# Performance work log

Hardware: AMD Instinct MI355X
Metric: run time of the kernel (lower is better)

Reference implementation:

```python
import jax, jax.numpy as jnp
import numpy as np

N_HEADS = 16
D_EMBED = 1024
D_CROSS = 768
D_HEAD = D_EMBED // N_HEADS
B, S = 4, 2048


def setup_inputs() -> dict:
    key = jax.random.key(0)
    ks = jax.random.split(key, 10)
    sq = lambda k, shp, fan: jax.random.normal(k, shp, jnp.float32) / np.sqrt(fan)
    return {
        "x": jax.random.normal(ks[0], (B, S, D_EMBED), jnp.float32),
        "y": jax.random.normal(ks[1], (B, S, D_CROSS), jnp.float32),
        "Wq": sq(ks[2], (D_EMBED, D_EMBED), D_EMBED),
        "bq": jnp.zeros((D_EMBED,), jnp.float32),
        "Wk": sq(ks[3], (D_CROSS, D_EMBED), D_CROSS),
        "bk": jnp.zeros((D_EMBED,), jnp.float32),
        "Wv": sq(ks[4], (D_CROSS, D_EMBED), D_CROSS),
        "bv": jnp.zeros((D_EMBED,), jnp.float32),
        "Wo": sq(ks[5], (D_EMBED, D_EMBED), D_EMBED),
        "bo": jnp.zeros((D_EMBED,), jnp.float32),
    }


def reference(x, y, Wq, bq, Wk, bk, Wv, bv, Wo, bo):
    b, s, _ = y.shape
    q = x @ Wq + bq  # [b, s, d_embed]
    k = y @ Wk + bk
    v = y @ Wv + bv
    # [b, h, s, d_head]
    q = q.reshape(b, s, N_HEADS, D_HEAD).transpose(0, 2, 1, 3)
    k = k.reshape(b, s, N_HEADS, D_HEAD).transpose(0, 2, 1, 3)
    v = v.reshape(b, s, N_HEADS, D_HEAD).transpose(0, 2, 1, 3)
    scale = 1.0 / np.sqrt(D_HEAD).astype(np.float32)
    scores = jnp.einsum("bhqd,bhkd->bhqk", q, k) * scale
    weights = jax.nn.softmax(scores, axis=-1)
    out = jnp.einsum("bhqk,bhkd->bhqd", weights, v)
    out = out.transpose(0, 2, 1, 3).reshape(x.shape)
    return out @ Wo + bo
```

## Files before the change

kernel.cpp:

```cpp
#include <hip/hip_runtime.h>

#define NHEADS 16
#define DEMBED 1024
#define DCROSS 768
#define DHEAD  64
#define BATCH  4
#define SLEN   2048
#define MROWS  (BATCH * SLEN)

using bf16   = __bf16;
using bf16x8 = __attribute__((ext_vector_type(8))) __bf16;
using bf16x4 = __attribute__((ext_vector_type(4))) __bf16;
using bf16x2 = __attribute__((ext_vector_type(2))) __bf16;
using f32x4  = __attribute__((ext_vector_type(4))) float;
using f32x16 = __attribute__((ext_vector_type(16))) float;

__device__ __forceinline__ f32x4 mfma_bf16(bf16x8 a, bf16x8 b, f32x4 c) {
    return __builtin_amdgcn_mfma_f32_16x16x32_bf16(a, b, c, 0, 0, 0);
}
__device__ __forceinline__ f32x16 mfma32(bf16x8 a, bf16x8 b, f32x16 c) {
    return __builtin_amdgcn_mfma_f32_32x32x16_bf16(a, b, c, 0, 0, 0);
}

__device__ __forceinline__ void gl2lds16(const void* g, void* l) {
    __builtin_amdgcn_global_load_lds(
        (const __attribute__((address_space(1))) void*)g,
        (__attribute__((address_space(3))) void*)l, 16, 0, 0);
}

struct PrepArgs {
    const float* wsrc[4]; bf16* wdst[4]; int wK[4];
    const float *x, *y; bf16 *xb, *yb;
};
#define NTRB 4096
__global__ void prep_all(PrepArgs a) {
    const int bid = blockIdx.x;
    const int tid = threadIdx.x;
    if (bid < NTRB) {
        __shared__ float tile[32][33];
        const int which = bid >> 10, rem = bid & 1023;
        const int K = a.wK[which], N = DEMBED;
        const int n0 = (rem & 31) * 32, k0 = (rem >> 5) * 32;
        if (k0 >= K) return;
        const float* W = a.wsrc[which];
        bf16* Wt = a.wdst[which];
        const int tx = tid & 31, ty = tid >> 5;
#pragma unroll
        for (int i = 0; i < 32; i += 8)
            tile[ty + i][tx] = W[(size_t)(k0 + ty + i) * N + n0 + tx];
        __syncthreads();
#pragma unroll
        for (int i = 0; i < 32; i += 8)
            Wt[(size_t)(n0 + ty + i) * K + k0 + tx] = (bf16)tile[tx][ty + i];
    } else {
        const int n4x = MROWS * DEMBED / 4;
        const int n4y = MROWS * DCROSS / 4;
        int i = (bid - NTRB) * 256 + tid;
        const float* src; bf16* dst; int j;
        if (i < n4x) { src = a.x; dst = a.xb; j = i; }
        else { j = i - n4x; if (j >= n4y) return; src = a.y; dst = a.yb; }
        float4 v = ((const float4*)src)[j];
        bf16x4 o = { (bf16)v.x, (bf16)v.y, (bf16)v.z, (bf16)v.w };
        ((bf16x4*)dst)[j] = o;
    }
}

struct QkvArgs {
    const bf16 *xb, *yb, *Wqt, *Wkt, *Wvt;
    const float *bq, *bk, *bv;
    bf16 *Qb, *Kb, *Vt;
    float qscale;
};
__global__ __launch_bounds__(256, 3) void gemm_qkv(QkvArgs a) {
    __shared__ bf16 As[128 * 64];
    __shared__ bf16 Bs[128 * 64];
    const int id = blockIdx.x;
    const int cls = id >> 9;
    const bf16 *A, *Bt;
    const float* bias;
    int K, m0, n0;
    if (cls == 0) { int t = id;        m0 = (t >> 3) * 128; n0 = (t & 7) * 128;
                    A = a.xb;  Bt = a.Wqt; bias = a.bq; K = DEMBED; }
    else if (cls == 1) { int t = id - 512;  m0 = (t >> 3) * 128; n0 = (t & 7) * 128;
                    A = a.yb;  Bt = a.Wkt; bias = a.bk; K = DCROSS; }
    else { int t = id - 1024; m0 = (t >> 6) * 128; n0 = (t & 63) * 128;
                    A = a.Wvt; Bt = a.yb;  bias = a.bv; K = DCROSS; }

    const int tid  = threadIdx.x;
    const int wave = tid >> 6, lane = tid & 63;
    const int quad = lane >> 4, l15 = lane & 15;
    const int wr = wave >> 1, wc = wave & 1;

    const int srow = wave * 8 + (lane >> 3);
    const int scol = ((lane & 7) ^ (lane >> 3)) * 8;
    char* ldsA0 = (char*)As + wave * 1024;
    char* ldsB0 = (char*)Bs + wave * 1024;
    const bf16* gA0 = A + (size_t)(m0 + srow) * K + scol;
    const bf16* gB0 = Bt + (size_t)(n0 + srow) * K + scol;

    const int sw = l15 & 7;

    f32x4 acc[4][4] = {};

    for (int kt = 0; kt < K; kt += 64) {
        __syncthreads();
#pragma unroll
        for (int c = 0; c < 4; c++)
            gl2lds16(gA0 + (size_t)c * 32 * K + kt, ldsA0 + c * 4096);
#pragma unroll
        for (int c = 0; c < 4; c++)
            gl2lds16(gB0 + (size_t)c * 32 * K + kt, ldsB0 + c * 4096);
        __syncthreads();

#pragma unroll
        for (int kg = 0; kg < 2; kg++) {
            bf16x8 af[4], bfr[4];
#pragma unroll
            for (int i = 0; i < 4; i++)
                af[i] = *(const bf16x8*)((const char*)As +
                         (wr * 64 + i * 16 + l15) * 128 + (((kg * 4 + quad) ^ sw) * 16));
#pragma unroll
            for (int i = 0; i < 4; i++)
                bfr[i] = *(const bf16x8*)((const char*)Bs +
                         (wc * 64 + i * 16 + l15) * 128 + (((kg * 4 + quad) ^ sw) * 16));
#pragma unroll
            for (int fr = 0; fr < 4; fr++)
#pragma unroll
                for (int fc = 0; fc < 4; fc++)
                    acc[fr][fc] = mfma_bf16(af[fr], bfr[fc], acc[fr][fc]);
        }
    }

    if (cls < 2) {
        bf16* Cout = (cls == 0) ? a.Qb : a.Kb;
        const float alpha = (cls == 0) ? a.qscale : 1.0f;
#pragma unroll
        for (int fr = 0; fr < 4; fr++) {
            int row = m0 + wr * 64 + fr * 16 + quad * 4;
#pragma unroll
            for (int fc = 0; fc < 4; fc++) {
                int col = n0 + wc * 64 + fc * 16 + l15;
                float bv = bias[col];
#pragma unroll
                for (int r = 0; r < 4; r++)
                    Cout[(size_t)(row + r) * DEMBED + col] =
                        (bf16)((acc[fr][fc][r] + bv) * alpha);
            }
        }
    } else {
        const int b = n0 >> 11;
        const size_t bbase = (size_t)b * DEMBED * SLEN;
#pragma unroll
        for (int fr = 0; fr < 4; fr++) {
            int row = m0 + wr * 64 + fr * 16 + quad * 4;
#pragma unroll
            for (int fc = 0; fc < 4; fc++) {
                int col = n0 + wc * 64 + fc * 16 + l15;
                int s = col & (SLEN - 1);
#pragma unroll
                for (int r = 0; r < 4; r++)
                    a.Vt[bbase + (size_t)(row + r) * SLEN + s] =
                        (bf16)(acc[fr][fc][r] + bias[row + r]);
            }
        }
    }
}

__global__ __launch_bounds__(256, 3) void gemm_o(const bf16* __restrict__ A,
                                                 const bf16* __restrict__ Bt,
                                                 const float* __restrict__ bias,
                                                 float* __restrict__ Cout) {
    const int K = DEMBED, N = DEMBED;
    __shared__ bf16 As[128 * 64];
    __shared__ bf16 Bs[128 * 64];
    const int tid  = threadIdx.x;
    const int wave = tid >> 6, lane = tid & 63;
    const int quad = lane >> 4, l15 = lane & 15;
    const int m0 = blockIdx.x * 128, n0 = blockIdx.y * 128;
    const int wr = wave >> 1, wc = wave & 1;

    const int srow = wave * 8 + (lane >> 3);
    const int scol = ((lane & 7) ^ (lane >> 3)) * 8;
    char* ldsA0 = (char*)As + wave * 1024;
    char* ldsB0 = (char*)Bs + wave * 1024;
    const bf16* gA0 = A + (size_t)(m0 + srow) * K + scol;
    const bf16* gB0 = Bt + (size_t)(n0 + srow) * K + scol;

    const int sw = l15 & 7;

    f32x4 acc[4][4] = {};

    for (int kt = 0; kt < K; kt += 64) {
        __syncthreads();
#pragma unroll
        for (int c = 0; c < 4; c++)
            gl2lds16(gA0 + (size_t)c * 32 * K + kt, ldsA0 + c * 4096);
#pragma unroll
        for (int c = 0; c < 4; c++)
            gl2lds16(gB0 + (size_t)c * 32 * K + kt, ldsB0 + c * 4096);
        __syncthreads();

#pragma unroll
        for (int kg = 0; kg < 2; kg++) {
            bf16x8 af[4], bfr[4];
#pragma unroll
            for (int i = 0; i < 4; i++)
                af[i] = *(const bf16x8*)((const char*)As +
                         (wr * 64 + i * 16 + l15) * 128 + (((kg * 4 + quad) ^ sw) * 16));
#pragma unroll
            for (int i = 0; i < 4; i++)
                bfr[i] = *(const bf16x8*)((const char*)Bs +
                         (wc * 64 + i * 16 + l15) * 128 + (((kg * 4 + quad) ^ sw) * 16));
#pragma unroll
            for (int fr = 0; fr < 4; fr++)
#pragma unroll
                for (int fc = 0; fc < 4; fc++)
                    acc[fr][fc] = mfma_bf16(af[fr], bfr[fc], acc[fr][fc]);
        }
    }

#pragma unroll
    for (int fr = 0; fr < 4; fr++) {
        int row = m0 + wr * 64 + fr * 16 + quad * 4;
#pragma unroll
        for (int fc = 0; fc < 4; fc++) {
            int col = n0 + wc * 64 + fc * 16 + l15;
            float bv = bias[col];
#pragma unroll
            for (int r = 0; r < 4; r++)
                Cout[(size_t)(row + r) * N + col] = acc[fr][fc][r] + bv;
        }
    }
}

__global__ __launch_bounds__(256, 4) void attn(const bf16* __restrict__ Q,
                                               const bf16* __restrict__ K,
                                               const bf16* __restrict__ Vt,
                                               bf16* __restrict__ O) {
    __shared__ bf16 KsA[2][64 * 64];
    __shared__ bf16 VsA[2][64 * 64];

    const int tid  = threadIdx.x;
    const int wave = tid >> 6, lane = tid & 63;
    const int l31  = lane & 31, H = lane >> 5;
    const int bh = blockIdx.x, b = bh >> 4, h = bh & 15;
    const size_t rowbase = (size_t)b * SLEN;
    const int qb = blockIdx.y * 128 + wave * 32;
    const int hc = h * DHEAD;

    bf16x8 qf[4];
#pragma unroll
    for (int ks = 0; ks < 4; ks++)
        qf[ks] = *(const bf16x8*)(Q + (rowbase + qb + l31) * DEMBED
                                  + hc + ks * 16 + H * 8);

    f32x16 o[2] = {};
    float lsv = 0.0f;

    const bf16* Kbase = K + rowbase * DEMBED + hc;
    const bf16* Vbase = Vt + (size_t)bh * DHEAD * SLEN;

    const int xcol = (((tid & 7) ^ ((tid >> 3) & 7)) * 8);
    const bf16* gK = Kbase + (size_t)(tid >> 3) * DEMBED + xcol;
    const bf16* gV = Vbase + (size_t)(tid >> 3) * SLEN + xcol;

    const int swz = l31 & 7;

    {
        char* lk = (char*)KsA + wave * 1024;
        char* lv = (char*)VsA + wave * 1024;
        gl2lds16(gK, lk);
        gl2lds16(gK + (size_t)32 * DEMBED, lk + 32 * 128);
        gl2lds16(gV, lv);
        gl2lds16(gV + 32 * SLEN, lv + 32 * 128);
    }
    __syncthreads();

    int cur = 0;
    for (int kb = 0; kb < SLEN; kb += 64) {
        if (kb + 64 < SLEN) {
            char* lk = (char*)KsA + (cur ^ 1) * 8192 + wave * 1024;
            char* lv = (char*)VsA + (cur ^ 1) * 8192 + wave * 1024;
            gl2lds16(gK + (size_t)(kb + 64) * DEMBED, lk);
            gl2lds16(gK + (size_t)(kb + 96) * DEMBED, lk + 32 * 128);
            gl2lds16(gV + kb + 64, lv);
            gl2lds16(gV + 32 * SLEN + kb + 64, lv + 32 * 128);
        }

        const char* Kbuf = (const char*)KsA + cur * 8192;
        const char* Vbuf = (const char*)VsA + cur * 8192;

        f32x16 s0 = {}, s1 = {};
#pragma unroll
        for (int ks = 0; ks < 4; ks++) {
            bf16x8 kf0 = *(const bf16x8*)(Kbuf + l31 * 128
                          + (((2 * ks + H) ^ swz) * 16));
            bf16x8 kf1 = *(const bf16x8*)(Kbuf + (32 + l31) * 128
                          + (((2 * ks + H) ^ swz) * 16));
            s0 = mfma32(kf0, qf[ks], s0);
            s1 = mfma32(kf1, qf[ks], s1);
        }

        int c0[8], c1[8];
#pragma unroll
        for (int t = 0; t < 8; t++) {
            float a0 = __builtin_amdgcn_exp2f(s0[2 * t]);
            float a1 = __builtin_amdgcn_exp2f(s0[2 * t + 1]);
            float b0 = __builtin_amdgcn_exp2f(s1[2 * t]);
            float b1 = __builtin_amdgcn_exp2f(s1[2 * t + 1]);
            lsv += (a0 + a1) + (b0 + b1);
            union { bf16x2 h; int i; } p0, p1;
            p0.h[0] = (bf16)a0; p0.h[1] = (bf16)a1;
            p1.h[0] = (bf16)b0; p1.h[1] = (bf16)b1;
            c0[t] = p0.i;
            c1[t] = p1.i;
        }

#pragma unroll
        for (int ks = 0; ks < 4; ks++) {
            const int* cc = (ks < 2) ? c0 : c1;
            const int ksl = ks & 1;
            auto w0 = __builtin_amdgcn_permlane32_swap(cc[4 * ksl + 0],
                                                       cc[4 * ksl + 2], false, false);
            auto w1 = __builtin_amdgcn_permlane32_swap(cc[4 * ksl + 1],
                                                       cc[4 * ksl + 3], false, false);
            union { int i[4]; bf16x8 v; } ap;
            ap.i[0] = w0[0]; ap.i[1] = w1[0]; ap.i[2] = w0[1]; ap.i[3] = w1[1];
#pragma unroll
            for (int dg = 0; dg < 2; dg++) {
                bf16x8 vf = *(const bf16x8*)(Vbuf + (dg * 32 + l31) * 128
                              + (((2 * ks + H) ^ swz) * 16));
                o[dg] = mfma32(ap.v, vf, o[dg]);
            }
        }

        __syncthreads();
        cur ^= 1;
    }

    lsv += __shfl_xor(lsv, 32);
    float inv = 1.0f / lsv;
#pragma unroll
    for (int r = 0; r < 16; r++) {
        const int ql = (r & 3) + 8 * (r >> 2) + 4 * H;
        float iv = __shfl(inv, ql);
#pragma unroll
        for (int dg = 0; dg < 2; dg++)
            O[(rowbase + qb + ql) * DEMBED + hc + dg * 32 + l31] =
                (bf16)(o[dg][r] * iv);
    }
}

extern "C" void kernel_launch(void* const* d_in, const int* in_sizes, int n_in,
                              void* d_out, int out_size, void* d_ws, size_t ws_size,
                              hipStream_t stream) {
    const float* x  = (const float*)d_in[0];
    const float* y  = (const float*)d_in[1];
    const float* Wq = (const float*)d_in[2];
    const float* bq = (const float*)d_in[3];
    const float* Wk = (const float*)d_in[4];
    const float* bk = (const float*)d_in[5];
    const float* Wv = (const float*)d_in[6];
    const float* bv = (const float*)d_in[7];
    const float* Wo = (const float*)d_in[8];
    const float* bo = (const float*)d_in[9];
    float* out = (float*)d_out;

    char* ws = (char*)d_ws;
    size_t off = 0;
    auto alloc = [&](size_t bytes) {
        void* p = ws + off;
        off += (bytes + 255) & ~(size_t)255;
        return p;
    };
    bf16* xb  = (bf16*)alloc((size_t)MROWS * DEMBED * 2);
    bf16* yb  = (bf16*)alloc((size_t)MROWS * DCROSS * 2);
    bf16* Wqt = (bf16*)alloc((size_t)DEMBED * DEMBED * 2);
    bf16* Wkt = (bf16*)alloc((size_t)DEMBED * DCROSS * 2);
    bf16* Wvt = (bf16*)alloc((size_t)DEMBED * DCROSS * 2);
    bf16* Wot = (bf16*)alloc((size_t)DEMBED * DEMBED * 2);
    bf16* Qb  = (bf16*)alloc((size_t)MROWS * DEMBED * 2);
    bf16* Kb  = (bf16*)alloc((size_t)MROWS * DEMBED * 2);
    bf16* Vtb = (bf16*)alloc((size_t)MROWS * DEMBED * 2);
    bf16* Ab  = (bf16*)alloc((size_t)MROWS * DEMBED * 2);
    if (off > ws_size) return;

    {
        PrepArgs a;
        a.wsrc[0] = Wq; a.wdst[0] = Wqt; a.wK[0] = DEMBED;
        a.wsrc[1] = Wk; a.wdst[1] = Wkt; a.wK[1] = DCROSS;
        a.wsrc[2] = Wv; a.wdst[2] = Wvt; a.wK[2] = DCROSS;
        a.wsrc[3] = Wo; a.wdst[3] = Wot; a.wK[3] = DEMBED;
        a.x = x; a.y = y; a.xb = xb; a.yb = yb;
        int ncvt = (MROWS * DEMBED / 4 + MROWS * DCROSS / 4 + 255) / 256;
        prep_all<<<NTRB + ncvt, 256, 0, stream>>>(a);
    }

    {
        QkvArgs a;
        a.xb = xb; a.yb = yb; a.Wqt = Wqt; a.Wkt = Wkt; a.Wvt = Wvt;
        a.bq = bq; a.bk = bk; a.bv = bv;
        a.Qb = Qb; a.Kb = Kb; a.Vt = Vtb;
        a.qscale = 0.125f * 1.4426950408889634f;
        gemm_qkv<<<1536, 256, 0, stream>>>(a);
    }

    attn<<<dim3(BATCH * NHEADS, SLEN / 128), 256, 0, stream>>>(Qb, Kb, Vtb, Ab);

    gemm_o<<<dim3(MROWS / 128, DEMBED / 128), 256, 0, stream>>>(Ab, Wot, bo, out);
}
```

Measured before the change: 277.3 us.

## Process 64 query rows per wave in attention, halving waves per block

The attention kernel now launches 128-thread blocks in which each wave handles two 32-row query sub-tiles instead of one. Every K and V fragment read from LDS is reused across both sub-tiles, which halves LDS reads per MFMA. The K/V staging loop is rewritten so two waves load the whole 64x64 tile. s_setprio hints are placed around the MFMA sections. The cost is roughly double the accumulator and score registers per wave and fewer waves per block, so occupancy and latency hiding may drop.

```diff
diff --git a/kernel.cpp b/kernel.cpp
--- a/kernel.cpp
+++ b/kernel.cpp
@@ -233,7 +233,7 @@
     }
 }
 
-__global__ __launch_bounds__(256, 4) void attn(const bf16* __restrict__ Q,
+__global__ __launch_bounds__(128, 2) void attn(const bf16* __restrict__ Q,
                                                const bf16* __restrict__ K,
                                                const bf16* __restrict__ Vt,
                                                bf16* __restrict__ O) {
@@ -245,92 +245,114 @@
     const int l31  = lane & 31, H = lane >> 5;
     const int bh = blockIdx.x, b = bh >> 4, h = bh & 15;
     const size_t rowbase = (size_t)b * SLEN;
-    const int qb = blockIdx.y * 128 + wave * 32;
+    const int qb = blockIdx.y * 128 + wave * 64;
     const int hc = h * DHEAD;
 
-    bf16x8 qf[4];
-#pragma unroll
-    for (int ks = 0; ks < 4; ks++)
-        qf[ks] = *(const bf16x8*)(Q + (rowbase + qb + l31) * DEMBED
-                                  + hc + ks * 16 + H * 8);
-
-    f32x16 o[2] = {};
-    float lsv = 0.0f;
+    bf16x8 qf[2][4];
+#pragma unroll
+    for (int qs = 0; qs < 2; qs++)
+#pragma unroll
+        for (int ks = 0; ks < 4; ks++)
+            qf[qs][ks] = *(const bf16x8*)(Q + (rowbase + qb + qs * 32 + l31) * DEMBED
+                                          + hc + ks * 16 + H * 8);
+
+    f32x16 o00 = {}, o01 = {}, o10 = {}, o11 = {};
+    float lsv0 = 0.0f, lsv1 = 0.0f;
 
     const bf16* Kbase = K + rowbase * DEMBED + hc;
     const bf16* Vbase = Vt + (size_t)bh * DHEAD * SLEN;
 
-    const int xcol = (((tid & 7) ^ ((tid >> 3) & 7)) * 8);
-    const bf16* gK = Kbase + (size_t)(tid >> 3) * DEMBED + xcol;
-    const bf16* gV = Vbase + (size_t)(tid >> 3) * SLEN + xcol;
+    const int grow = tid >> 3;
+    const int xcol = ((tid & 7) ^ (grow & 7)) * 8;
+    const bf16* gK = Kbase + (size_t)grow * DEMBED + xcol;
+    const bf16* gV = Vbase + (size_t)grow * SLEN + xcol;
 
     const int swz = l31 & 7;
 
-    {
-        char* lk = (char*)KsA + wave * 1024;
-        char* lv = (char*)VsA + wave * 1024;
-        gl2lds16(gK, lk);
-        gl2lds16(gK + (size_t)32 * DEMBED, lk + 32 * 128);
-        gl2lds16(gV, lv);
-        gl2lds16(gV + 32 * SLEN, lv + 32 * 128);
-    }
+    auto STAGE = [&](int buf, int kb) {
+        char* lk = (char*)KsA + buf * 8192 + wave * 1024;
+        char* lv = (char*)VsA + buf * 8192 + wave * 1024;
+#pragma unroll
+        for (int c = 0; c < 4; c++) {
+            gl2lds16(gK + (size_t)(kb + c * 16) * DEMBED, lk + c * 2048);
+            gl2lds16(gV + (size_t)(c * 16) * SLEN + kb,   lv + c * 2048);
+        }
+    };
+
+    STAGE(0, 0);
     __syncthreads();
 
     int cur = 0;
     for (int kb = 0; kb < SLEN; kb += 64) {
-        if (kb + 64 < SLEN) {
-            char* lk = (char*)KsA + (cur ^ 1) * 8192 + wave * 1024;
-            char* lv = (char*)VsA + (cur ^ 1) * 8192 + wave * 1024;
-            gl2lds16(gK + (size_t)(kb + 64) * DEMBED, lk);
-            gl2lds16(gK + (size_t)(kb + 96) * DEMBED, lk + 32 * 128);
-            gl2lds16(gV + kb + 64, lv);
-            gl2lds16(gV + 32 * SLEN + kb + 64, lv + 32 * 128);
-        }
+        if (kb + 64 < SLEN) STAGE(cur ^ 1, kb + 64);
 
         const char* Kbuf = (const char*)KsA + cur * 8192;
         const char* Vbuf = (const char*)VsA + cur * 8192;
 
-        f32x16 s0 = {}, s1 = {};
+        f32x16 s00 = {}, s01 = {}, s10 = {}, s11 = {};
+        __builtin_amdgcn_s_setprio(1);
 #pragma unroll
         for (int ks = 0; ks < 4; ks++) {
-            bf16x8 kf0 = *(const bf16x8*)(Kbuf + l31 * 128
-                          + (((2 * ks + H) ^ swz) * 16));
-            bf16x8 kf1 = *(const bf16x8*)(Kbuf + (32 + l31) * 128
-                          + (((2 * ks + H) ^ swz) * 16));
-            s0 = mfma32(kf0, qf[ks], s0);
-            s1 = mfma32(kf1, qf[ks], s1);
-        }
-
-        int c0[8], c1[8];
+            const int slot = ((2 * ks + H) ^ swz) * 16;
+            bf16x8 kf0 = *(const bf16x8*)(Kbuf + l31 * 128 + slot);
+            bf16x8 kf1 = *(const bf16x8*)(Kbuf + (32 + l31) * 128 + slot);
+            s00 = mfma32(kf0, qf[0][ks], s00);
+            s01 = mfma32(kf1, qf[0][ks], s01);
+            s10 = mfma32(kf0, qf[1][ks], s10);
+            s11 = mfma32(kf1, qf[1][ks], s11);
+        }
+        __builtin_amdgcn_s_setprio(0);
+
+        int cA0[8], cB0[8], cA1[8], cB1[8];
 #pragma unroll
         for (int t = 0; t < 8; t++) {
-            float a0 = __builtin_amdgcn_exp2f(s0[2 * t]);
-            float a1 = __builtin_amdgcn_exp2f(s0[2 * t + 1]);
-            float b0 = __builtin_amdgcn_exp2f(s1[2 * t]);
-            float b1 = __builtin_amdgcn_exp2f(s1[2 * t + 1]);
-            lsv += (a0 + a1) + (b0 + b1);
+            float a0 = __builtin_amdgcn_exp2f(s00[2 * t]);
+            float a1 = __builtin_amdgcn_exp2f(s00[2 * t + 1]);
+            float b0 = __builtin_amdgcn_exp2f(s01[2 * t]);
+            float b1 = __builtin_amdgcn_exp2f(s01[2 * t + 1]);
+            lsv0 += (a0 + a1) + (b0 + b1);
             union { bf16x2 h; int i; } p0, p1;
             p0.h[0] = (bf16)a0; p0.h[1] = (bf16)a1;
             p1.h[0] = (bf16)b0; p1.h[1] = (bf16)b1;
-            c0[t] = p0.i;
-            c1[t] = p1.i;
-        }
-
-#pragma unroll
-        for (int ks = 0; ks < 4; ks++) {
-            const int* cc = (ks < 2) ? c0 : c1;
-            const int ksl = ks & 1;
+            cA0[t] = p0.i;
+            cB0[t] = p1.i;
+            float c0 = __builtin_amdgcn_exp2f(s10[2 * t]);
+            float c1 = __builtin_amdgcn_exp2f(s10[2 * t + 1]);
+            float d0 = __builtin_amdgcn_exp2f(s11[2 * t]);
+            float d1 = __builtin_amdgcn_exp2f(s11[2 * t + 1]);
+            lsv1 += (c0 + c1) + (d0 + d1);
+            union { bf16x2 h; int i; } p2, p3;
+            p2.h[0] = (bf16)c0; p2.h[1] = (bf16)c1;
+            p3.h[0] = (bf16)d0; p3.h[1] = (bf16)d1;
+            cA1[t] = p2.i;
+            cB1[t] = p3.i;
+        }
+
+        auto pvpair = [&](const int* cc, int ksl, bf16x8 vf0, bf16x8 vf1,
+                          f32x16& oo0, f32x16& oo1) {
             auto w0 = __builtin_amdgcn_permlane32_swap(cc[4 * ksl + 0],
                                                        cc[4 * ksl + 2], false, false);
             auto w1 = __builtin_amdgcn_permlane32_swap(cc[4 * ksl + 1],
                                                        cc[4 * ksl + 3], false, false);
             union { int i[4]; bf16x8 v; } ap;
             ap.i[0] = w0[0]; ap.i[1] = w1[0]; ap.i[2] = w0[1]; ap.i[3] = w1[1];
-#pragma unroll
-            for (int dg = 0; dg < 2; dg++) {
-                bf16x8 vf = *(const bf16x8*)(Vbuf + (dg * 32 + l31) * 128
-                              + (((2 * ks + H) ^ swz) * 16));
-                o[dg] = mfma32(ap.v, vf, o[dg]);
+            __builtin_amdgcn_s_setprio(1);
+            oo0 = mfma32(ap.v, vf0, oo0);
+            oo1 = mfma32(ap.v, vf1, oo1);
+            __builtin_amdgcn_s_setprio(0);
+        };
+#pragma unroll
+        for (int ks = 0; ks < 4; ks++) {
+            const int slot = ((2 * ks + H) ^ swz) * 16;
+            bf16x8 vf0 = *(const bf16x8*)(Vbuf + l31 * 128 + slot);
+            bf16x8 vf1 = *(const bf16x8*)(Vbuf + (32 + l31) * 128 + slot);
+            const int ksl = ks & 1;
+            if (ks < 2) {
+                pvpair(cA0, ksl, vf0, vf1, o00, o01);
+                pvpair(cA1, ksl, vf0, vf1, o10, o11);
+            } else {
+                pvpair(cB0, ksl, vf0, vf1, o00, o01);
+                pvpair(cB1, ksl, vf0, vf1, o10, o11);
             }
         }
 
@@ -338,16 +360,19 @@
         cur ^= 1;
     }
 
-    lsv += __shfl_xor(lsv, 32);
-    float inv = 1.0f / lsv;
+    lsv0 += __shfl_xor(lsv0, 32);
+    lsv1 += __shfl_xor(lsv1, 32);
+    float inv0 = 1.0f / lsv0;
+    float inv1 = 1.0f / lsv1;
 #pragma unroll
     for (int r = 0; r < 16; r++) {
         const int ql = (r & 3) + 8 * (r >> 2) + 4 * H;
-        float iv = __shfl(inv, ql);
-#pragma unroll
-        for (int dg = 0; dg < 2; dg++)
-            O[(rowbase + qb + ql) * DEMBED + hc + dg * 32 + l31] =
-                (bf16)(o[dg][r] * iv);
+        float iv0 = __shfl(inv0, ql);
+        float iv1 = __shfl(inv1, ql);
+        O[(rowbase + qb + ql) * DEMBED + hc + l31]      = (bf16)(o00[r] * iv0);
+        O[(rowbase + qb + ql) * DEMBED + hc + 32 + l31] = (bf16)(o01[r] * iv0);
+        O[(rowbase + qb + 32 + ql) * DEMBED + hc + l31]      = (bf16)(o10[r] * iv1);
+        O[(rowbase + qb + 32 + ql) * DEMBED + hc + 32 + l31] = (bf16)(o11[r] * iv1);
     }
 }
 
@@ -405,7 +430,7 @@
         gemm_qkv<<<1536, 256, 0, stream>>>(a);
     }
 
-    attn<<<dim3(BATCH * NHEADS, SLEN / 128), 256, 0, stream>>>(Qb, Kb, Vtb, Ab);
+    attn<<<dim3(BATCH * NHEADS, SLEN / 128), 128, 0, stream>>>(Qb, Kb, Vtb, Ab);
 
     gemm_o<<<dim3(MROWS / 128, DEMBED / 128), 256, 0, stream>>>(Ab, Wot, bo, out);
 }
```

After: 280.3 us. About the same (+1.1%).

## Triple-buffer QKV GEMM with 256x128 tiles, 512 threads and XCD-aware block remap

Applied to the files above, without the earlier changes.

Rewrites the QKV projection GEMM to use 512-thread blocks computing 256x128 tiles. A three-stage LDS ring buffer issues global-to-LDS loads two K-tiles ahead, gated by explicit vmcnt waits instead of two full barriers per step. It also adds MFMA priority raising and remaps block IDs so neighbouring tiles land on the same XCD for L2 reuse. The gain should come from hiding load latency and reusing the B tile across more rows. The cost is larger LDS use (144 KB per block), which limits occupancy, and a fragile hand-tuned wait count.

```diff
diff --git a/kernel.cpp b/kernel.cpp
--- a/kernel.cpp
+++ b/kernel.cpp
@@ -71,64 +71,92 @@
     bf16 *Qb, *Kb, *Vt;
     float qscale;
 };
-__global__ __launch_bounds__(256, 3) void gemm_qkv(QkvArgs a) {
-    __shared__ bf16 As[128 * 64];
-    __shared__ bf16 Bs[128 * 64];
-    const int id = blockIdx.x;
-    const int cls = id >> 9;
+__global__ __launch_bounds__(512, 2) void gemm_qkv(QkvArgs a) {
+    __shared__ bf16 As[3 * 256 * 64];
+    __shared__ bf16 Bs[3 * 128 * 64];
+    const int rb  = blockIdx.x;
+    const int bid = (rb & 7) * 96 + (rb >> 3);
+    const int cls = bid >> 8;
+    const int tt  = bid & 255;
     const bf16 *A, *Bt;
     const float* bias;
     int K, m0, n0;
-    if (cls == 0) { int t = id;        m0 = (t >> 3) * 128; n0 = (t & 7) * 128;
-                    A = a.xb;  Bt = a.Wqt; bias = a.bq; K = DEMBED; }
-    else if (cls == 1) { int t = id - 512;  m0 = (t >> 3) * 128; n0 = (t & 7) * 128;
-                    A = a.yb;  Bt = a.Wkt; bias = a.bk; K = DCROSS; }
-    else { int t = id - 1024; m0 = (t >> 6) * 128; n0 = (t & 63) * 128;
-                    A = a.Wvt; Bt = a.yb;  bias = a.bv; K = DCROSS; }
+    if (cls == 0)      { m0 = (tt >> 3) << 8; n0 = (tt & 7) << 7;
+                         A = a.xb;  Bt = a.Wqt; bias = a.bq; K = DEMBED; }
+    else if (cls == 1) { m0 = (tt >> 3) << 8; n0 = (tt & 7) << 7;
+                         A = a.yb;  Bt = a.Wkt; bias = a.bk; K = DCROSS; }
+    else               { m0 = (tt >> 6) << 8; n0 = (tt & 63) << 7;
+                         A = a.Wvt; Bt = a.yb;  bias = a.bv; K = DCROSS; }
 
     const int tid  = threadIdx.x;
     const int wave = tid >> 6, lane = tid & 63;
     const int quad = lane >> 4, l15 = lane & 15;
     const int wr = wave >> 1, wc = wave & 1;
 
-    const int srow = wave * 8 + (lane >> 3);
-    const int scol = ((lane & 7) ^ (lane >> 3)) * 8;
-    char* ldsA0 = (char*)As + wave * 1024;
-    char* ldsB0 = (char*)Bs + wave * 1024;
-    const bf16* gA0 = A + (size_t)(m0 + srow) * K + scol;
-    const bf16* gB0 = Bt + (size_t)(n0 + srow) * K + scol;
+    const int srow = tid >> 3;
+    const int gcol = ((tid & 7) ^ (srow & 7)) * 8;
+    char* ldsA = (char*)As + wave * 1024;
+    char* ldsB = (char*)Bs + wave * 1024;
+    const bf16* gA0 = A + (size_t)(m0 + srow) * K + gcol;
+    const bf16* gB0 = Bt + (size_t)(n0 + srow) * K + gcol;
 
     const int sw = l15 & 7;
+    const int NT = K >> 6;
+
+    auto STAGE = [&](int buf, int kt) {
+        char* la = ldsA + buf * 32768;
+        char* lb = ldsB + buf * 16384;
+#pragma unroll
+        for (int c = 0; c < 4; c++)
+            gl2lds16(gA0 + (size_t)c * 64 * K + kt, la + c * 8192);
+#pragma unroll
+        for (int c = 0; c < 2; c++)
+            gl2lds16(gB0 + (size_t)c * 64 * K + kt, lb + c * 8192);
+    };
 
     f32x4 acc[4][4] = {};
 
-    for (int kt = 0; kt < K; kt += 64) {
-        __syncthreads();
-#pragma unroll
-        for (int c = 0; c < 4; c++)
-            gl2lds16(gA0 + (size_t)c * 32 * K + kt, ldsA0 + c * 4096);
-#pragma unroll
-        for (int c = 0; c < 4; c++)
-            gl2lds16(gB0 + (size_t)c * 32 * K + kt, ldsB0 + c * 4096);
-        __syncthreads();
-
+    STAGE(0, 0);
+    STAGE(1, 64);
+
+    int buf = 0;
+    for (int t2 = 0; t2 < NT; ++t2) {
+        if (t2 + 2 < NT) STAGE(buf == 0 ? 2 : buf - 1, (t2 + 2) << 6);
+        const int rem = NT - 1 - t2;
+        if (rem >= 2)      asm volatile("s_waitcnt vmcnt(12)");
+        else if (rem == 1) asm volatile("s_waitcnt vmcnt(6)");
+        else               asm volatile("s_waitcnt vmcnt(0)");
+        __builtin_amdgcn_sched_barrier(0);
+        __builtin_amdgcn_s_barrier();
+        __builtin_amdgcn_sched_barrier(0);
+
+        const char* Ab = (const char*)As + buf * 32768;
+        const char* Bb = (const char*)Bs + buf * 16384;
 #pragma unroll
         for (int kg = 0; kg < 2; kg++) {
             bf16x8 af[4], bfr[4];
 #pragma unroll
             for (int i = 0; i < 4; i++)
-                af[i] = *(const bf16x8*)((const char*)As +
+                bfr[i] = *(const bf16x8*)(Bb +
+                         (wc * 64 + i * 16 + l15) * 128 + (((kg * 4 + quad) ^ sw) * 16));
+#pragma unroll
+            for (int i = 0; i < 4; i++)
+                af[i] = *(const bf16x8*)(Ab +
                          (wr * 64 + i * 16 + l15) * 128 + (((kg * 4 + quad) ^ sw) * 16));
-#pragma unroll
-            for (int i = 0; i < 4; i++)
-                bfr[i] = *(const bf16x8*)((const char*)Bs +
-                         (wc * 64 + i * 16 + l15) * 128 + (((kg * 4 + quad) ^ sw) * 16));
+            __builtin_amdgcn_s_setprio(1);
 #pragma unroll
             for (int fr = 0; fr < 4; fr++)
 #pragma unroll
                 for (int fc = 0; fc < 4; fc++)
                     acc[fr][fc] = mfma_bf16(af[fr], bfr[fc], acc[fr][fc]);
-        }
+            __builtin_amdgcn_s_setprio(0);
+        }
+
+        asm volatile("s_waitcnt lgkmcnt(0)");
+        __builtin_amdgcn_sched_barrier(0);
+        __builtin_amdgcn_s_barrier();
+        __builtin_amdgcn_sched_barrier(0);
+        buf = (buf == 2) ? 0 : buf + 1;
     }
 
     if (cls < 2) {
@@ -402,7 +430,7 @@
         a.bq = bq; a.bk = bk; a.bv = bv;
         a.Qb = Qb; a.Kb = Kb; a.Vt = Vtb;
         a.qscale = 0.125f * 1.4426950408889634f;
-        gemm_qkv<<<1536, 256, 0, stream>>>(a);
+        gemm_qkv<<<768, 512, 0, stream>>>(a);
     }
 
     attn<<<dim3(BATCH * NHEADS, SLEN / 128), 256, 0, stream>>>(Qb, Kb, Vtb, Ab);
```

Result: slower. 298.5 us (+7.6%).
